# Performance work log

Measured on AMD Instinct MI355X. Metric: run time of the kernel, lower is better.

Reference implementation:

```python
import jax, jax.numpy as jnp
import numpy as np

B, IN_DIM, HID, ATT = 16384, 128, 512, 256
TOTAL = IN_DIM + HID + ATT


def setup_inputs() -> dict:
    key = jax.random.key(0)
    ks = jax.random.split(key, 10)
    u = lambda k, shape, lo, hi: jax.random.uniform(k, shape, jnp.float32, lo, hi)
    return {
        "t": jnp.float32(0.0),
        "h_ltc": jax.random.normal(ks[0], (B, HID), jnp.float32),
        "x_t": jax.random.normal(ks[1], (B, IN_DIM), jnp.float32),
        "context": jax.random.normal(ks[2], (B, ATT), jnp.float32),
        "W_gd": u(ks[3], (2 * HID, TOTAL), -0.1, 0.1),
        "b_gd": u(ks[4], (2 * HID,), -0.1, 0.1),
        "W_tau": u(ks[5], (HID, HID), -0.1, 0.1),
        "b_tau": u(ks[6], (HID,), -0.1, 0.1),
        "gleak": u(ks[7], (HID,), 0.001, 1.0),
        "cm": u(ks[8], (HID,), 0.4, 0.6),
    }


def reference(t, h_ltc, x_t, context, W_gd, b_gd, W_tau, b_tau, gleak, cm):
    # combined: [B, IN+HID+ATT]
    combined = jnp.concatenate([x_t, h_ltc, context], axis=1)
    g_d = combined @ W_gd.T + b_gd            # [B, 2*HID]
    gate, dynamics = jnp.split(g_d, 2, axis=1)
    tau = jax.nn.softplus(h_ltc @ W_tau.T + b_tau)  # [B, HID]
    numerator = jax.nn.sigmoid(gate) * jnp.tanh(dynamics) - h_ltc
    denominator = tau + jax.nn.softplus(cm) + jax.nn.softplus(gleak)
    return numerator / (denominator + 1e-6)
```

## Files before the change

kernel.cpp:

```cpp
#include <hip/hip_runtime.h>
#include <hip/hip_bf16.h>
#include <math.h>

#define BROWS 16384
#define IN_DIM 128
#define HID 512
#define ATT 256
#define KTOT 896
#define KC_TOT 112

typedef __bf16 bf16x8 __attribute__((ext_vector_type(8)));
typedef float f32x4 __attribute__((ext_vector_type(4)));

__device__ __forceinline__ float softplus_f(float x) {
    return fmaxf(x, 0.0f) + log1pf(__expf(-fabsf(x)));
}

__global__ void pack_B(const float* __restrict__ W_gd, const float* __restrict__ W_tau,
                       const float* __restrict__ gleak, const float* __restrict__ cm,
                       __hip_bfloat16* __restrict__ B_stage, float* __restrict__ dconst) {
    const int cid = blockIdx.x * 256 + threadIdx.x;
    if (cid < HID) {
        dconst[cid] = softplus_f(cm[cid]) + softplus_f(gleak[cid]) + 1e-6f;
    }
    const int nl = cid % 192;
    const int kc = (cid / 192) % KC_TOT;
    const int jt = cid / (192 * KC_TOT);
    const int jg = nl / 48, type = (nl % 48) / 16, j16 = nl % 16;
    const int j = jt * 64 + jg * 16 + j16;
    const int k0 = kc * 8;

    float v[8];
    if (type == 0) {
        const float* s = W_gd + (size_t)j * KTOT + k0;
        #pragma unroll
        for (int i = 0; i < 8; ++i) v[i] = s[i];
    } else if (type == 1) {
        const float* s = W_gd + (size_t)(HID + j) * KTOT + k0;
        #pragma unroll
        for (int i = 0; i < 8; ++i) v[i] = s[i];
    } else {
        if (k0 >= IN_DIM && k0 < IN_DIM + HID) {
            const float* s = W_tau + (size_t)j * HID + (k0 - IN_DIM);
            #pragma unroll
            for (int i = 0; i < 8; ++i) v[i] = s[i];
        } else {
            #pragma unroll
            for (int i = 0; i < 8; ++i) v[i] = 0.0f;
        }
    }
    union { __hip_bfloat16 hh[8]; uint4 u; } p;
    #pragma unroll
    for (int i = 0; i < 8; ++i) p.hh[i] = __float2bfloat16(v[i]);
    *(uint4*)(B_stage + (size_t)cid * 8) = p.u;
}

__global__ __launch_bounds__(512, 4) void ltc_gemm(
    const float* __restrict__ x, const float* __restrict__ h_ltc,
    const float* __restrict__ ctx, const __hip_bfloat16* __restrict__ B_stage,
    const float* __restrict__ b_gd, const float* __restrict__ b_tau,
    const float* __restrict__ dconst, float* __restrict__ out) {

    __shared__ __attribute__((aligned(16))) char As[57344];

    const int mt = blockIdx.x;
    const int tid = threadIdx.x;
    const int wave = tid >> 6, lane = tid & 63;
    const int q = lane >> 4, t = lane & 15;

    const int mi = tid >> 4;
    const int kcg = tid & 15;
    #pragma unroll
    for (int s = 0; s < 7; ++s) {
        const int kc = kcg + 16 * s;
        const float* src; int rs, col;
        if (s == 0)      { src = x;     rs = IN_DIM; col = kcg * 8; }
        else if (s < 5)  { src = h_ltc; rs = HID;    col = kcg * 8 + (s - 1) * 128; }
        else             { src = ctx;   rs = ATT;    col = kcg * 8 + (s - 5) * 128; }
        const float* p = src + (size_t)(mt * 32 + mi) * rs + col;
        float4 v0 = *(const float4*)p;
        float4 v1 = *(const float4*)(p + 4);
        union { __hip_bfloat16 hh[8]; uint4 u; } pk;
        pk.hh[0] = __float2bfloat16(v0.x); pk.hh[1] = __float2bfloat16(v0.y);
        pk.hh[2] = __float2bfloat16(v0.z); pk.hh[3] = __float2bfloat16(v0.w);
        pk.hh[4] = __float2bfloat16(v1.x); pk.hh[5] = __float2bfloat16(v1.y);
        pk.hh[6] = __float2bfloat16(v1.z); pk.hh[7] = __float2bfloat16(v1.w);
        *(uint4*)(As + ((kc * 32 + (mi ^ (kc & 31))) << 4)) = pk.u;
    }
    __syncthreads();

    for (int it = 0; it < 4; ++it) {
        const int jglob = it * 128 + wave * 16;
        const int jt = jglob >> 6;
        const int jg = (jglob >> 4) & 3;
        const __hip_bfloat16* bBase = B_stage
            + ((size_t)jt * (KC_TOT * 192) + jg * 48 + t) * 8;

        f32x4 acc[2][3];
        #pragma unroll
        for (int f = 0; f < 2; ++f)
            #pragma unroll
            for (int ty = 0; ty < 3; ++ty) acc[f][ty] = (f32x4)0.0f;

        bf16x8 ab[2][2]; bf16x8 bb[2][3];

        {
            const int kc = q;
            ab[0][0] = *(const bf16x8*)(As + ((kc * 32 + (t ^ kc)) << 4));
            ab[0][1] = *(const bf16x8*)(As + ((kc * 32 + ((16 + t) ^ kc)) << 4));
            const __hip_bfloat16* bp = bBase + (size_t)kc * 1536;
            bb[0][0] = *(const bf16x8*)(bp);
            bb[0][1] = *(const bf16x8*)(bp + 128);
        }

        #pragma unroll 4
        for (int kst = 0; kst < 28; ++kst) {
            const int cb = kst & 1, nb = cb ^ 1;
            const bool tau_cur = (kst >= 4 && kst < 20);
            if (kst < 27) {
                const int kc = (kst + 1) * 4 + q;
                const int sw = kc & 31;
                ab[nb][0] = *(const bf16x8*)(As + ((kc * 32 + (t ^ sw)) << 4));
                ab[nb][1] = *(const bf16x8*)(As + ((kc * 32 + ((16 + t) ^ sw)) << 4));
                const __hip_bfloat16* bp = bBase + (size_t)kc * 1536;
                bb[nb][0] = *(const bf16x8*)(bp);
                bb[nb][1] = *(const bf16x8*)(bp + 128);
                if (kst + 1 >= 4 && kst + 1 < 20)
                    bb[nb][2] = *(const bf16x8*)(bp + 256);
            }
            acc[0][0] = __builtin_amdgcn_mfma_f32_16x16x32_bf16(ab[cb][0], bb[cb][0], acc[0][0], 0, 0, 0);
            acc[1][0] = __builtin_amdgcn_mfma_f32_16x16x32_bf16(ab[cb][1], bb[cb][0], acc[1][0], 0, 0, 0);
            acc[0][1] = __builtin_amdgcn_mfma_f32_16x16x32_bf16(ab[cb][0], bb[cb][1], acc[0][1], 0, 0, 0);
            acc[1][1] = __builtin_amdgcn_mfma_f32_16x16x32_bf16(ab[cb][1], bb[cb][1], acc[1][1], 0, 0, 0);
            if (tau_cur) {
                acc[0][2] = __builtin_amdgcn_mfma_f32_16x16x32_bf16(ab[cb][0], bb[cb][2], acc[0][2], 0, 0, 0);
                acc[1][2] = __builtin_amdgcn_mfma_f32_16x16x32_bf16(ab[cb][1], bb[cb][2], acc[1][2], 0, 0, 0);
            }
        }

        const int j = jglob + t;
        const float bgj = b_gd[j];
        const float bdj = b_gd[HID + j];
        const float btj = b_tau[j];
        const float dcj = dconst[j];
        #pragma unroll
        for (int f = 0; f < 2; ++f) {
            #pragma unroll
            for (int r = 0; r < 4; ++r) {
                const int row = mt * 32 + f * 16 + q * 4 + r;
                const float gv = acc[f][0][r] + bgj;
                const float dv = acc[f][1][r] + bdj;
                const float tp = acc[f][2][r] + btj;
                const float hv = h_ltc[(size_t)row * HID + j];
                const float sig = __builtin_amdgcn_rcpf(1.0f + __expf(-gv));
                const float th  = 1.0f - 2.0f * __builtin_amdgcn_rcpf(__expf(2.0f * dv) + 1.0f);
                const float tau = fmaxf(tp, 0.0f) + __logf(1.0f + __expf(-fabsf(tp)));
                out[(size_t)row * HID + j] = (sig * th - hv) * __builtin_amdgcn_rcpf(tau + dcj);
            }
        }
    }
}

extern "C" void kernel_launch(void* const* d_in, const int* in_sizes, int n_in,
                              void* d_out, int out_size, void* d_ws, size_t ws_size,
                              hipStream_t stream) {
    const float* h_ltc = (const float*)d_in[1];
    const float* x_t   = (const float*)d_in[2];
    const float* ctx   = (const float*)d_in[3];
    const float* W_gd  = (const float*)d_in[4];
    const float* b_gd  = (const float*)d_in[5];
    const float* W_tau = (const float*)d_in[6];
    const float* b_tau = (const float*)d_in[7];
    const float* gleak = (const float*)d_in[8];
    const float* cm    = (const float*)d_in[9];

    char* ws = (char*)d_ws;
    __hip_bfloat16* B_stage = (__hip_bfloat16*)ws;
    float* dconst = (float*)(ws + 2752512);

    pack_B<<<672, 256, 0, stream>>>(W_gd, W_tau, gleak, cm, B_stage, dconst);
    ltc_gemm<<<512, 512, 0, stream>>>(x_t, h_ltc, ctx, B_stage, b_gd, b_tau, dconst,
                                      (float*)d_out);
}
```

Measured before the change: 162.8 us.

## Retile GEMM to 64-row by 128-column blocks with double-buffered K-slab staging

Each block now computes 64 rows by one 128-column quarter of the hidden output, instead of 32 rows by all 512 columns. The grid is 1024 blocks, mapped so that each XCD handles a contiguous set of row tiles. Activations are staged into LDS in 128-wide K slabs with double buffering, so global loads of the next slab overlap the MFMA work on the current one. Each B fragment is reused across four row fragments. In exchange, activations are re-read by four blocks, and the larger accumulator set raises register use, which lowers occupancy (launch bounds 2).

```diff
diff --git a/kernel.cpp b/kernel.cpp
--- a/kernel.cpp
+++ b/kernel.cpp
@@ -55,108 +55,125 @@
     *(uint4*)(B_stage + (size_t)cid * 8) = p.u;
 }
 
-__global__ __launch_bounds__(512, 4) void ltc_gemm(
+__global__ __launch_bounds__(512, 2) void ltc_gemm(
     const float* __restrict__ x, const float* __restrict__ h_ltc,
     const float* __restrict__ ctx, const __hip_bfloat16* __restrict__ B_stage,
     const float* __restrict__ b_gd, const float* __restrict__ b_tau,
     const float* __restrict__ dconst, float* __restrict__ out) {
 
-    __shared__ __attribute__((aligned(16))) char As[57344];
-
-    const int mt = blockIdx.x;
+    __shared__ __attribute__((aligned(16))) char As[2][16384];
+
+    const int wgid = blockIdx.x;
+    const int xcd = wgid & 7;
+    const int idx = wgid >> 3;
+    const int rt  = xcd * 32 + (idx >> 2);
+    const int jq  = idx & 3;
+
     const int tid = threadIdx.x;
     const int wave = tid >> 6, lane = tid & 63;
     const int q = lane >> 4, t = lane & 15;
 
-    const int mi = tid >> 4;
-    const int kcg = tid & 15;
+    const int srow = tid >> 3;
+    const int skc  = (tid & 7) * 2;
+
+    float4 av[4];
+
+    #define LOADW(w_) do {                                                        \
+        const float* _src; int _rs, _c0;                                          \
+        if ((w_) == 0)      { _src = x;     _rs = IN_DIM; _c0 = 0; }              \
+        else if ((w_) < 5)  { _src = h_ltc; _rs = HID;    _c0 = ((w_)-1)*128; }   \
+        else                { _src = ctx;   _rs = ATT;    _c0 = ((w_)-5)*128; }   \
+        const float* _p = _src + (size_t)(rt*64 + srow)*_rs + _c0 + skc*8;        \
+        av[0] = ((const float4*)_p)[0]; av[1] = ((const float4*)_p)[1];           \
+        av[2] = ((const float4*)_p)[2]; av[3] = ((const float4*)_p)[3];           \
+    } while (0)
+
+    #define WRITEW(buf_, w_) do {                                                 \
+        _Pragma("unroll")                                                         \
+        for (int _c = 0; _c < 2; ++_c) {                                          \
+            const int _kcl = skc + _c;                                            \
+            const int _sw = (((w_)*16) + _kcl) & 31;                              \
+            union { __hip_bfloat16 hh[8]; uint4 u; } _pk;                         \
+            const float4 _lo = av[_c*2], _hi = av[_c*2+1];                        \
+            _pk.hh[0]=__float2bfloat16(_lo.x); _pk.hh[1]=__float2bfloat16(_lo.y); \
+            _pk.hh[2]=__float2bfloat16(_lo.z); _pk.hh[3]=__float2bfloat16(_lo.w); \
+            _pk.hh[4]=__float2bfloat16(_hi.x); _pk.hh[5]=__float2bfloat16(_hi.y); \
+            _pk.hh[6]=__float2bfloat16(_hi.z); _pk.hh[7]=__float2bfloat16(_hi.w); \
+            *(uint4*)(&As[buf_][ ((_kcl*64) + (srow ^ _sw)) << 4 ]) = _pk.u;      \
+        }                                                                         \
+    } while (0)
+
+    const int jglob = jq * 128 + wave * 16;
+    const int jt = jglob >> 6;
+    const int jg = (jglob >> 4) & 3;
+    const __hip_bfloat16* bBase = B_stage
+        + ((size_t)jt * (KC_TOT * 192) + jg * 48 + t) * 8;
+
+    f32x4 acc[4][3];
     #pragma unroll
-    for (int s = 0; s < 7; ++s) {
-        const int kc = kcg + 16 * s;
-        const float* src; int rs, col;
-        if (s == 0)      { src = x;     rs = IN_DIM; col = kcg * 8; }
-        else if (s < 5)  { src = h_ltc; rs = HID;    col = kcg * 8 + (s - 1) * 128; }
-        else             { src = ctx;   rs = ATT;    col = kcg * 8 + (s - 5) * 128; }
-        const float* p = src + (size_t)(mt * 32 + mi) * rs + col;
-        float4 v0 = *(const float4*)p;
-        float4 v1 = *(const float4*)(p + 4);
-        union { __hip_bfloat16 hh[8]; uint4 u; } pk;
-        pk.hh[0] = __float2bfloat16(v0.x); pk.hh[1] = __float2bfloat16(v0.y);
-        pk.hh[2] = __float2bfloat16(v0.z); pk.hh[3] = __float2bfloat16(v0.w);
-        pk.hh[4] = __float2bfloat16(v1.x); pk.hh[5] = __float2bfloat16(v1.y);
-        pk.hh[6] = __float2bfloat16(v1.z); pk.hh[7] = __float2bfloat16(v1.w);
-        *(uint4*)(As + ((kc * 32 + (mi ^ (kc & 31))) << 4)) = pk.u;
-    }
+    for (int rf = 0; rf < 4; ++rf)
+        #pragma unroll
+        for (int ty = 0; ty < 3; ++ty) acc[rf][ty] = (f32x4)0.0f;
+
+    LOADW(0);
+    WRITEW(0, 0);
     __syncthreads();
 
-    for (int it = 0; it < 4; ++it) {
-        const int jglob = it * 128 + wave * 16;
-        const int jt = jglob >> 6;
-        const int jg = (jglob >> 4) & 3;
-        const __hip_bfloat16* bBase = B_stage
-            + ((size_t)jt * (KC_TOT * 192) + jg * 48 + t) * 8;
-
-        f32x4 acc[2][3];
-        #pragma unroll
-        for (int f = 0; f < 2; ++f)
-            #pragma unroll
-            for (int ty = 0; ty < 3; ++ty) acc[f][ty] = (f32x4)0.0f;
-
-        bf16x8 ab[2][2]; bf16x8 bb[2][3];
-
-        {
-            const int kc = q;
-            ab[0][0] = *(const bf16x8*)(As + ((kc * 32 + (t ^ kc)) << 4));
-            ab[0][1] = *(const bf16x8*)(As + ((kc * 32 + ((16 + t) ^ kc)) << 4));
+    for (int w = 0; w < 7; ++w) {
+        const int cb = w & 1;
+        if (w < 6) LOADW(w + 1);
+        const bool tau_cur = (w >= 1 && w <= 4);
+        const char* Ab = As[cb];
+        #pragma unroll
+        for (int s = 0; s < 4; ++s) {
+            const int kc  = w * 16 + s * 4 + q;
+            const int kcl = s * 4 + q;
+            const int sw  = kc & 31;
+            const bf16x8 a0 = *(const bf16x8*)(Ab + ((kcl*64 + ( t        ^ sw)) << 4));
+            const bf16x8 a1 = *(const bf16x8*)(Ab + ((kcl*64 + ((16 + t)  ^ sw)) << 4));
+            const bf16x8 a2 = *(const bf16x8*)(Ab + ((kcl*64 + ((32 + t)  ^ sw)) << 4));
+            const bf16x8 a3 = *(const bf16x8*)(Ab + ((kcl*64 + ((48 + t)  ^ sw)) << 4));
             const __hip_bfloat16* bp = bBase + (size_t)kc * 1536;
-            bb[0][0] = *(const bf16x8*)(bp);
-            bb[0][1] = *(const bf16x8*)(bp + 128);
-        }
-
-        #pragma unroll 4
-        for (int kst = 0; kst < 28; ++kst) {
-            const int cb = kst & 1, nb = cb ^ 1;
-            const bool tau_cur = (kst >= 4 && kst < 20);
-            if (kst < 27) {
-                const int kc = (kst + 1) * 4 + q;
-                const int sw = kc & 31;
-                ab[nb][0] = *(const bf16x8*)(As + ((kc * 32 + (t ^ sw)) << 4));
-                ab[nb][1] = *(const bf16x8*)(As + ((kc * 32 + ((16 + t) ^ sw)) << 4));
-                const __hip_bfloat16* bp = bBase + (size_t)kc * 1536;
-                bb[nb][0] = *(const bf16x8*)(bp);
-                bb[nb][1] = *(const bf16x8*)(bp + 128);
-                if (kst + 1 >= 4 && kst + 1 < 20)
-                    bb[nb][2] = *(const bf16x8*)(bp + 256);
-            }
-            acc[0][0] = __builtin_amdgcn_mfma_f32_16x16x32_bf16(ab[cb][0], bb[cb][0], acc[0][0], 0, 0, 0);
-            acc[1][0] = __builtin_amdgcn_mfma_f32_16x16x32_bf16(ab[cb][1], bb[cb][0], acc[1][0], 0, 0, 0);
-            acc[0][1] = __builtin_amdgcn_mfma_f32_16x16x32_bf16(ab[cb][0], bb[cb][1], acc[0][1], 0, 0, 0);
-            acc[1][1] = __builtin_amdgcn_mfma_f32_16x16x32_bf16(ab[cb][1], bb[cb][1], acc[1][1], 0, 0, 0);
+            const bf16x8 bg = *(const bf16x8*)(bp);
+            const bf16x8 bd = *(const bf16x8*)(bp + 128);
+            acc[0][0] = __builtin_amdgcn_mfma_f32_16x16x32_bf16(a0, bg, acc[0][0], 0, 0, 0);
+            acc[1][0] = __builtin_amdgcn_mfma_f32_16x16x32_bf16(a1, bg, acc[1][0], 0, 0, 0);
+            acc[2][0] = __builtin_amdgcn_mfma_f32_16x16x32_bf16(a2, bg, acc[2][0], 0, 0, 0);
+            acc[3][0] = __builtin_amdgcn_mfma_f32_16x16x32_bf16(a3, bg, acc[3][0], 0, 0, 0);
+            acc[0][1] = __builtin_amdgcn_mfma_f32_16x16x32_bf16(a0, bd, acc[0][1], 0, 0, 0);
+            acc[1][1] = __builtin_amdgcn_mfma_f32_16x16x32_bf16(a1, bd, acc[1][1], 0, 0, 0);
+            acc[2][1] = __builtin_amdgcn_mfma_f32_16x16x32_bf16(a2, bd, acc[2][1], 0, 0, 0);
+            acc[3][1] = __builtin_amdgcn_mfma_f32_16x16x32_bf16(a3, bd, acc[3][1], 0, 0, 0);
             if (tau_cur) {
-                acc[0][2] = __builtin_amdgcn_mfma_f32_16x16x32_bf16(ab[cb][0], bb[cb][2], acc[0][2], 0, 0, 0);
-                acc[1][2] = __builtin_amdgcn_mfma_f32_16x16x32_bf16(ab[cb][1], bb[cb][2], acc[1][2], 0, 0, 0);
+                const bf16x8 bt = *(const bf16x8*)(bp + 256);
+                acc[0][2] = __builtin_amdgcn_mfma_f32_16x16x32_bf16(a0, bt, acc[0][2], 0, 0, 0);
+                acc[1][2] = __builtin_amdgcn_mfma_f32_16x16x32_bf16(a1, bt, acc[1][2], 0, 0, 0);
+                acc[2][2] = __builtin_amdgcn_mfma_f32_16x16x32_bf16(a2, bt, acc[2][2], 0, 0, 0);
+                acc[3][2] = __builtin_amdgcn_mfma_f32_16x16x32_bf16(a3, bt, acc[3][2], 0, 0, 0);
             }
         }
-
-        const int j = jglob + t;
-        const float bgj = b_gd[j];
-        const float bdj = b_gd[HID + j];
-        const float btj = b_tau[j];
-        const float dcj = dconst[j];
-        #pragma unroll
-        for (int f = 0; f < 2; ++f) {
-            #pragma unroll
-            for (int r = 0; r < 4; ++r) {
-                const int row = mt * 32 + f * 16 + q * 4 + r;
-                const float gv = acc[f][0][r] + bgj;
-                const float dv = acc[f][1][r] + bdj;
-                const float tp = acc[f][2][r] + btj;
-                const float hv = h_ltc[(size_t)row * HID + j];
-                const float sig = __builtin_amdgcn_rcpf(1.0f + __expf(-gv));
-                const float th  = 1.0f - 2.0f * __builtin_amdgcn_rcpf(__expf(2.0f * dv) + 1.0f);
-                const float tau = fmaxf(tp, 0.0f) + __logf(1.0f + __expf(-fabsf(tp)));
-                out[(size_t)row * HID + j] = (sig * th - hv) * __builtin_amdgcn_rcpf(tau + dcj);
-            }
+        if (w < 6) WRITEW(cb ^ 1, w + 1);
+        __syncthreads();
+    }
+
+    const int j = jglob + t;
+    const float bgj = b_gd[j];
+    const float bdj = b_gd[HID + j];
+    const float btj = b_tau[j];
+    const float dcj = dconst[j];
+    #pragma unroll
+    for (int rf = 0; rf < 4; ++rf) {
+        #pragma unroll
+        for (int r = 0; r < 4; ++r) {
+            const int row = rt * 64 + rf * 16 + q * 4 + r;
+            const float gv = acc[rf][0][r] + bgj;
+            const float dv = acc[rf][1][r] + bdj;
+            const float tp = acc[rf][2][r] + btj;
+            const float hv = h_ltc[(size_t)row * HID + j];
+            const float sig = __builtin_amdgcn_rcpf(1.0f + __expf(-gv));
+            const float th  = 1.0f - 2.0f * __builtin_amdgcn_rcpf(__expf(2.0f * dv) + 1.0f);
+            const float tau = fmaxf(tp, 0.0f) + __logf(1.0f + __expf(-fabsf(tp)));
+            out[(size_t)row * HID + j] = (sig * th - hv) * __builtin_amdgcn_rcpf(tau + dcj);
         }
     }
 }
@@ -179,6 +196,6 @@
     float* dconst = (float*)(ws + 2752512);
 
     pack_B<<<672, 256, 0, stream>>>(W_gd, W_tau, gleak, cm, B_stage, dconst);
-    ltc_gemm<<<512, 512, 0, stream>>>(x_t, h_ltc, ctx, B_stage, b_gd, b_tau, dconst,
-                                      (float*)d_out);
-}
+    ltc_gemm<<<1024, 512, 0, stream>>>(x_t, h_ltc, ctx, B_stage, b_gd, b_tau, dconst,
+                                       (float*)d_out);
+}
```

Measured after the change: 209.4 us. +28.6%, slower.
